# Optimization experiments

Measured on AMD Instinct MI355X. Metric: run time of the kernel, lower is better.

## Reference

```python
import math
import jax, jax.numpy as jnp
import numpy as np

B, T, D, V, S, R = 128, 32, 64, 4096, 32, 8
PONDER = 0.01
TWO_PI = np.float32(2.0 * math.pi)


def _ln(x, g, b, eps=1e-5):
    mu = x.mean(-1, keepdims=True)
    var = ((x - mu) ** 2).mean(-1, keepdims=True)
    return (x - mu) / jnp.sqrt(var + eps) * g + b


def _clin(xr, xi, Wr, br, Wi, bi):
    # ComplexLinear: fc_real/fc_imag share biases per torch module
    real = (xr @ Wr + br) - (xi @ Wi + bi)
    imag = (xi @ Wr + br) + (xr @ Wi + bi)
    return real, imag


def setup_inputs() -> dict:
    key = jax.random.key(0)
    ks = jax.random.split(key, 10)
    f = lambda k, sh, s: jax.random.normal(k, sh, jnp.float32) * s
    return {
        "x_seq": jax.random.randint(ks[0], (B, T), 0, V),
        "enc_emb": f(ks[1], (V, 2 * D), 0.02),
        "vq_emb": f(ks[2], (V, 2 * D), 0.05),
        "norm_rg": jnp.ones((D,), jnp.float32),
        "norm_rb": jnp.zeros((D,), jnp.float32),
        "norm_ig": jnp.ones((D,), jnp.float32),
        "norm_ib": jnp.zeros((D,), jnp.float32),
        "proj_w": f(ks[3], (3, 2, D, D), 0.05),  # [q/k/v, real/imag, in, out]
        "proj_b": f(ks[4], (3, 2, D), 0.01),
        "mem_gate_w": f(ks[5], (2 * D, 1), 0.05),
        "mem_gate_b": jnp.zeros((1,), jnp.float32),
        "arb_w": f(ks[6], (2 * D, 3), 0.05),
        "arb_b": jnp.zeros((3,), jnp.float32),
        "dec_w": f(ks[7], (2 * D, V), 0.02),
        "dec_b": jnp.zeros((V,), jnp.float32),
        "halt_bias": jnp.array(3.0, jnp.float32),
        "input_gate": jnp.array(0.0, jnp.float32),
    }


def _fwd(x_seq, enc_emb, vq_emb, norm_rg, norm_rb, norm_ig, norm_ib,
         proj_w, proj_b, mem_gate_w, mem_gate_b, arb_w, arb_b,
         dec_w, dec_b, halt_bias, input_gate):
    sg = jax.lax.stop_gradient
    emb = enc_emb[x_seq]                         # [B,T,2D]
    er, ei = emb[..., :D], emb[..., D:]
    alpha = jax.nn.sigmoid(input_gate)
    bias = jax.nn.softplus(halt_bias)
    vq_sq = (vq_emb ** 2).sum(-1)                # [V]

    def step(carry, xs):
        gw_r, gw_i, mem_r, mem_i = carry
        x_r, x_i = xs
        gw_r = alpha * gw_r + (1.0 - alpha) * x_r
        gw_i = alpha * gw_i + (1.0 - alpha) * x_i
        active = jnp.ones((x_r.shape[0],), jnp.float32)
        acc_vq = jnp.zeros_like(active)
        acc_ppx = jnp.zeros_like(active)
        acc_ent = jnp.zeros_like(active)
        acc_pond = jnp.zeros_like(active)
        acc_ph = jnp.zeros_like(active)
        prev_ang = jnp.arctan2(gw_i, gw_r)
        for _ in range(R):
            cr = _ln(gw_r, norm_rg, norm_rb)
            ci = _ln(gw_i, norm_ig, norm_ib)
            flat = jnp.concatenate([cr, ci], -1)            # [B,2D]
            # VQ (argmin over squared euclidean == argmin over cdist)
            d2 = (flat ** 2).sum(-1, keepdims=True) - 2.0 * (flat @ vq_emb.T) + vq_sq
            idx = jnp.argmin(d2, -1)                        # [B]
            zq = vq_emb[idx]                                # [B,2D]
            vq_loss = ((zq - sg(flat)) ** 2).mean(-1) + 0.25 * ((sg(zq) - flat) ** 2).mean(-1)
            zq_st = flat + sg(zq - flat)                    # straight-through
            avg = jax.nn.one_hot(idx, V, dtype=jnp.float32).mean(0)
            ent = -(avg * jnp.log(avg + 1e-10)).sum()
            ppx = jnp.exp(ent)
            vq_r, vq_i = zq_st[:, :D], zq_st[:, D:]
            # Hermitian gating
            qr, qi = _clin(cr, ci, proj_w[0, 0], proj_b[0, 0], proj_w[0, 1], proj_b[0, 1])
            kr, ki = _clin(cr, ci, proj_w[1, 0], proj_b[1, 0], proj_w[1, 1], proj_b[1, 1])
            wr, wi = _clin(cr, ci, proj_w[2, 0], proj_b[2, 0], proj_w[2, 1], proj_b[2, 1])
            gate = jax.nn.sigmoid((qr * kr + qi * ki).sum(-1, keepdims=True))
            g_r, g_i = wr * gate, wi * gate
            # memory read (mem unchanged during recursion)
            sim = jnp.einsum('bsd,bd->bs', mem_r, cr) + jnp.einsum('bsd,bd->bs', mem_i, ci)
            attn = jax.nn.softmax(sim, -1)
            m_r = jnp.einsum('bs,bsd->bd', attn, mem_r)
            m_i = jnp.einsum('bs,bsd->bd', attn, mem_i)
            # arbitrator mix
            gates = jax.nn.softmax(flat @ arb_w + arb_b, -1)  # [B,3]
            u_r = gates[:, 0:1] * g_r + gates[:, 1:2] * m_r + gates[:, 2:3] * vq_r
            u_i = gates[:, 0:1] * g_i + gates[:, 1:2] * m_i + gates[:, 2:3] * vq_i
            c_r = 0.6 * cr + 0.4 * u_r
            c_i = 0.6 * ci + 0.4 * u_i
            ang = jnp.arctan2(c_i, c_r)
            diff = jnp.abs(ang - prev_ang)
            diff = jnp.minimum(diff, TWO_PI - diff)
            acc_ph = acc_ph + active * diff.mean(-1)
            prev_ang = ang
            halt = jax.nn.sigmoid(bias - vq_loss)
            stop = (halt > 0.5).astype(jnp.float32)
            acc_pond = acc_pond + active * PONDER
            m = active > 0.5
            acc_vq = jnp.where(m, vq_loss, acc_vq)
            acc_ppx = jnp.where(m, ppx, acc_ppx)
            acc_ent = jnp.where(m, ent, acc_ent)
            gw_r = jnp.where(m[:, None], c_r, gw_r)
            gw_i = jnp.where(m[:, None], c_i, gw_i)
            active = active * (1.0 - stop)
        # final memory write (read output discarded, matching torch)
        flat_gw = jnp.concatenate([gw_r, gw_i], -1)
        wg = jax.nn.sigmoid(flat_gw @ mem_gate_w + mem_gate_b)  # [B,1]
        sh_r = jnp.roll(mem_r, 1, axis=1)
        sh_i = jnp.roll(mem_i, 1, axis=1)
        mem_r = sh_r.at[:, 0].set(wg * gw_r + (1.0 - wg) * sh_r[:, 0])
        mem_i = sh_i.at[:, 0].set(wg * gw_i + (1.0 - wg) * sh_i[:, 0])
        stats = jnp.stack([acc_vq.mean(), acc_ppx.mean(), acc_ent.mean(),
                           acc_pond.mean(), acc_ph.mean()])
        return (gw_r, gw_i, mem_r, mem_i), (gw_r, gw_i, stats)

    init = (jnp.zeros((B, D), jnp.float32), jnp.zeros((B, D), jnp.float32),
            jnp.zeros((B, S, D), jnp.float32), jnp.zeros((B, S, D), jnp.float32))
    xs = (jnp.moveaxis(er, 1, 0), jnp.moveaxis(ei, 1, 0))
    (gw_r, gw_i, mem_r, mem_i), (o_r, o_i, stats) = jax.lax.scan(step, init, xs)
    flat_out = jnp.concatenate([jnp.moveaxis(o_r, 0, 1), jnp.moveaxis(o_i, 0, 1)], -1)  # [B,T,2D]
    logits = flat_out @ dec_w + dec_b
    return logits, stats.mean(0), mem_r, mem_i


def reference(x_seq, enc_emb, vq_emb, norm_rg, norm_rb, norm_ig, norm_ib,
              proj_w, proj_b, mem_gate_w, mem_gate_b, arb_w, arb_b,
              dec_w, dec_b, halt_bias, input_gate):
    return _fwd(x_seq, enc_emb, vq_emb, norm_rg, norm_rb, norm_ig, norm_ib,
                proj_w, proj_b, mem_gate_w, mem_gate_b, arb_w, arb_b,
                dec_w, dec_b, halt_bias, input_gate)
```

## Files before the change

### kernel.cpp

```cpp
#include <hip/hip_runtime.h>
#include <math.h>

#define BB 128
#define TT 32
#define DDIM 64
#define VV 4096
#define SS 32
#define RR 8
#define NT 512
#define SMP 65

typedef unsigned short u16;
typedef unsigned int u32;
typedef _Float16 h2 __attribute__((ext_vector_type(2)));

__device__ __forceinline__ h2 bch(u32 u){ union { u32 u; h2 h; } v; v.u = u; return v.h; }

__device__ __forceinline__ float fdot2f(u32 a, u32 b, float acc){
#if __has_builtin(__builtin_amdgcn_fdot2)
  return __builtin_amdgcn_fdot2(bch(a), bch(b), acc, false);
#else
  h2 x = bch(a), y = bch(b);
  return acc + (float)x[0] * (float)y[0] + (float)x[1] * (float)y[1];
#endif
}

__device__ __forceinline__ u32 packh2(float a, float b){
  union { _Float16 h[2]; u32 u; } p;
  p.h[0] = (_Float16)a; p.h[1] = (_Float16)b;
  return p.u;
}

__global__ __launch_bounds__(256) void k_pack(const float* __restrict__ vq, u32* __restrict__ vqT){
  int gid = blockIdx.x * 256 + threadIdx.x;
  int l   = gid & 63;
  int dc8 = (gid >> 6) & 15;
  int c0  = gid >> 10;
  int c   = (c0 << 6) + l;
  const float* s = vq + c * 128 + dc8 * 8;
  uint4 o;
  o.x = packh2(s[0], s[1]);
  o.y = packh2(s[2], s[3]);
  o.z = packh2(s[4], s[5]);
  o.w = packh2(s[6], s[7]);
  ((uint4*)vqT)[gid] = o;
}

__global__ __launch_bounds__(256) void k_vqsq(const float* __restrict__ vq, float* __restrict__ vqsq){
  int c = blockIdx.x * 256 + threadIdx.x;
  float s = 0.f;
  for (int d = 0; d < 128; d++){ float v = vq[c * 128 + d]; s = fmaf(v, v, s); }
  vqsq[c] = s;
}

__global__ __launch_bounds__(NT) void k_recur(
    const int* __restrict__ x_seq, const float* __restrict__ enc_emb,
    const float* __restrict__ vq_emb, const u32* __restrict__ vqT,
    const float* __restrict__ vq_sq,
    const float* __restrict__ nrg, const float* __restrict__ nrb,
    const float* __restrict__ nig, const float* __restrict__ nib,
    const float* __restrict__ proj_w, const float* __restrict__ proj_b,
    const float* __restrict__ mgw, const float* __restrict__ mgb,
    const float* __restrict__ arb_w, const float* __restrict__ arb_b,
    const float* __restrict__ hb, const float* __restrict__ ig,
    float* __restrict__ gwout, float* __restrict__ flatF,
    int* __restrict__ idxbuf, int* __restrict__ rstop_g, float* __restrict__ accs,
    float* __restrict__ out_mem)
{
  const int b = blockIdx.x;
  const int tid = threadIdx.x;
  const int lane = tid & 63;
  const int wave = tid >> 6;

  __shared__ __align__(16) float s_gw[128];
  __shared__ __align__(16) float s_flat[128];
  __shared__ __align__(16) u32   s_flath[64];
  __shared__ float s_zq[128];
  __shared__ float s_c[128];
  __shared__ float s_mem[2][SS][SMP];
  __shared__ float s_mv[12][DDIM];
  __shared__ float s_qkw[6][DDIM];
  __shared__ float s_sim[SS];
  __shared__ float s_red[16];
  __shared__ float s_sc[4];
  __shared__ int   s_imin;
  __shared__ float s_cand[8];
  __shared__ int   s_candi[8];

  for (int i = tid; i < 128; i += NT) s_gw[i] = 0.f;
  for (int i = tid; i < 2 * SS * SMP; i += NT) ((float*)s_mem)[i] = 0.f;
  __syncthreads();

  const float alpha = 1.f / (1.f + expf(-ig[0]));
  float bias_h; { float x = hb[0]; bias_h = log1pf(expf(x)); }
  int head = 0;
  float prev_ang = 0.f;

  for (int t = 0; t < TT; t++){
    int xid = x_seq[b * TT + t];
    if (tid < 128){
      float e = enc_emb[xid * 128 + tid];
      s_gw[tid] = alpha * s_gw[tid] + (1.f - alpha) * e;
    }
    __syncthreads();
    if (wave == 0) prev_ang = atan2f(s_gw[64 + lane], s_gw[lane]);

    float acc_ph = 0.f, acc_vq = 0.f;
    int rst = 0;

    for (int r = 0; r < RR; r++){
      if (wave < 2){
        float x = s_gw[wave * 64 + lane];
        float mu = x;
        for (int m = 1; m < 64; m <<= 1) mu += __shfl_xor(mu, m);
        mu *= (1.f / 64.f);
        float dxl = x - mu;
        float vv = dxl * dxl;
        for (int m = 1; m < 64; m <<= 1) vv += __shfl_xor(vv, m);
        vv *= (1.f / 64.f);
        float rs = 1.f / sqrtf(vv + 1e-5f);
        const float* g  = wave ? nig : nrg;
        const float* bb = wave ? nib : nrb;
        float fv = dxl * rs * g[lane] + bb[lane];
        s_flat[wave * 64 + lane] = fv;
        float pv = __shfl_xor(fv, 1);
        if ((lane & 1) == 0)
          s_flath[(wave * 64 + lane) >> 1] = packh2(fv, pv);
      }
      __syncthreads();

      uint4 F[16];
      {
        const uint4* sfh4 = (const uint4*)s_flath;
        #pragma unroll
        for (int i = 0; i < 16; i++) F[i] = sfh4[i];
      }
      float bsc = 3.4e38f; int bidx = 0;
      #pragma unroll 1
      for (int k = 0; k < 8; k++){
        int c0 = wave + 8 * k;
        const uint4* vp = ((const uint4*)vqT) + (c0 * 16) * 64 + lane;
        uint4 U[16];
        #pragma unroll
        for (int dc8 = 0; dc8 < 16; dc8++) U[dc8] = vp[dc8 * 64];
        float dot = 0.f;
        #pragma unroll
        for (int dc8 = 0; dc8 < 16; dc8++){
          dot = fdot2f(U[dc8].x, F[dc8].x, dot);
          dot = fdot2f(U[dc8].y, F[dc8].y, dot);
          dot = fdot2f(U[dc8].z, F[dc8].z, dot);
          dot = fdot2f(U[dc8].w, F[dc8].w, dot);
        }
        int c = c0 * 64 + lane;
        float sc = vq_sq[c] - 2.f * dot;
        if (sc < bsc || (sc == bsc && c < bidx)){ bsc = sc; bidx = c; }
      }
      for (int m = 1; m < 64; m <<= 1){
        float os = __shfl_xor(bsc, m);
        int   oi = __shfl_xor(bidx, m);
        if (os < bsc || (os == bsc && oi < bidx)){ bsc = os; bidx = oi; }
      }
      if (lane == 0){ s_cand[wave] = bsc; s_candi[wave] = bidx; }
      __syncthreads();
      if (tid == 0){
        float bs = s_cand[0]; int bi = s_candi[0];
        for (int w = 1; w < 8; w++){
          float os = s_cand[w]; int oi = s_candi[w];
          if (os < bs || (os == bs && oi < bi)){ bs = os; bi = oi; }
        }
        s_imin = bi;
        idxbuf[(b * TT + t) * RR + r] = bi;
      }
      __syncthreads();
      int imin = s_imin;

      if (tid < 128){
        float z = vq_emb[imin * 128 + tid];
        s_zq[tid] = z;
        float dv = z - s_flat[tid];
        float sq = dv * dv;
        for (int m = 1; m < 64; m <<= 1) sq += __shfl_xor(sq, m);
        if (lane == 0) s_red[wave] = sq;
      }
      for (int mm = wave; mm < 12; mm += 8){
        int p = mm >> 2, kind = mm & 3;
        int xoff = (kind == 0 || kind == 3) ? 0 : 64;
        int wsel = (kind == 0 || kind == 2) ? 0 : 1;
        const float* W = proj_w + ((p * 2 + wsel) << 12);
        const float4* fx = (const float4*)&s_flat[xoff];
        float a = 0.f;
        #pragma unroll
        for (int i = 0; i < 16; i++){
          float4 fv = fx[i];
          a = fmaf(fv.x, W[(4 * i + 0) * 64 + lane], a);
          a = fmaf(fv.y, W[(4 * i + 1) * 64 + lane], a);
          a = fmaf(fv.z, W[(4 * i + 2) * 64 + lane], a);
          a = fmaf(fv.w, W[(4 * i + 3) * 64 + lane], a);
        }
        s_mv[mm][lane] = a;
      }
      __syncthreads();

      if (tid == 0) s_sc[1] = 1.25f * (s_red[0] + s_red[1]) * (1.f / 128.f);
      if (tid < 192){
        int p = tid >> 6, j = tid & 63;
        float A  = s_mv[p * 4 + 0][j];
        float Bv = s_mv[p * 4 + 1][j];
        float C  = s_mv[p * 4 + 2][j];
        float Dv = s_mv[p * 4 + 3][j];
        float br = proj_b[(p * 2 + 0) * 64 + j];
        float bi = proj_b[(p * 2 + 1) * 64 + j];
        s_qkw[p * 2 + 0][j] = A + br - Bv - bi;
        s_qkw[p * 2 + 1][j] = C + br + Dv + bi;
      }
      __syncthreads();

      if (wave == 0){
        float g = s_qkw[0][lane] * s_qkw[2][lane] + s_qkw[1][lane] * s_qkw[3][lane];
        for (int m = 1; m < 64; m <<= 1) g += __shfl_xor(g, m);
        if (lane == 0) s_sc[0] = 1.f / (1.f + expf(-g));
      }
      {
        int slot = tid >> 4, sub = tid & 15;
        float p = 0.f;
        for (int k = 0; k < 8; k++){
          int dd = sub * 8 + k;
          float mv = (dd < 64) ? s_mem[0][slot][dd] : s_mem[1][slot][dd - 64];
          p = fmaf(mv, s_flat[dd], p);
        }
        for (int m = 1; m < 16; m <<= 1) p += __shfl_xor(p, m, 16);
        if (sub == 0) s_sim[slot] = p;
      }
      __syncthreads();
      if (wave == 0 && lane < 32){
        float v = s_sim[lane];
        float mx = v;
        for (int m = 1; m < 32; m <<= 1) mx = fmaxf(mx, __shfl_xor(mx, m, 32));
        float e = expf(v - mx);
        float sm = e;
        for (int m = 1; m < 32; m <<= 1) sm += __shfl_xor(sm, m, 32);
        s_sim[lane] = e / sm;
      }
      __syncthreads();
      float m_reg = 0.f;
      if (tid < 128){
        int h = tid >> 6, d0 = tid & 63;
        for (int s2 = 0; s2 < 32; s2++)
          m_reg = fmaf(s_sim[s2], s_mem[h][s2][d0], m_reg);
      } else if (wave >= 2 && wave < 5){
        int k = wave - 2;
        float p = s_flat[lane] * arb_w[lane * 3 + k]
                + s_flat[64 + lane] * arb_w[(64 + lane) * 3 + k];
        for (int m = 1; m < 64; m <<= 1) p += __shfl_xor(p, m);
        if (lane == 0) s_red[4 + k] = p + arb_b[k];
      }
      __syncthreads();
      if (tid < 128){
        float l0 = s_red[4], l1 = s_red[5], l2 = s_red[6];
        float mx = fmaxf(l0, fmaxf(l1, l2));
        float e0 = expf(l0 - mx), e1 = expf(l1 - mx), e2 = expf(l2 - mx);
        float inv = 1.f / (e0 + e1 + e2);
        float g0 = e0 * inv, g1 = e1 * inv, g2 = e2 * inv;
        float gate = s_sc[0];
        int h = tid >> 6, j = tid & 63;
        float wv = s_qkw[4 + h][j];
        float u = g0 * (gate * wv) + g1 * m_reg + g2 * s_zq[tid];
        s_c[tid] = 0.6f * s_flat[tid] + 0.4f * u;
      }
      __syncthreads();
      if (wave == 0){
        float ang = atan2f(s_c[64 + lane], s_c[lane]);
        float df = fabsf(ang - prev_ang);
        df = fminf(df, 6.28318530717958647692f - df);
        prev_ang = ang;
        for (int m = 1; m < 64; m <<= 1) df += __shfl_xor(df, m);
        if (lane == 0) s_red[7] = df * (1.f / 64.f);
      }
      __syncthreads();
      float vl = s_sc[1];
      acc_ph += s_red[7];
      acc_vq = vl;
      rst = r;
      bool stop = (bias_h - vl) > 0.f;
      if (tid < 128) s_gw[tid] = s_c[tid];
      __syncthreads();
      if (stop) break;
    }

    float pond = 0.01f * (float)(rst + 1);
    if (tid < 128) gwout[(b * TT + t) * 128 + tid] = s_gw[tid];
    if (rst < RR - 1 && wave < 2){
      float x = s_gw[wave * 64 + lane];
      float mu = x;
      for (int m = 1; m < 64; m <<= 1) mu += __shfl_xor(mu, m);
      mu *= (1.f / 64.f);
      float dxl = x - mu;
      float vv = dxl * dxl;
      for (int m = 1; m < 64; m <<= 1) vv += __shfl_xor(vv, m);
      vv *= (1.f / 64.f);
      float rs = 1.f / sqrtf(vv + 1e-5f);
      const float* g  = wave ? nig : nrg;
      const float* bb = wave ? nib : nrb;
      flatF[(b * TT + t) * 128 + wave * 64 + lane] = dxl * rs * g[lane] + bb[lane];
    }
    if (wave < 2){
      float p = s_gw[wave * 64 + lane] * mgw[wave * 64 + lane];
      for (int m = 1; m < 64; m <<= 1) p += __shfl_xor(p, m);
      if (lane == 0) s_red[8 + wave] = p;
    }
    __syncthreads();
    float wg = 1.f / (1.f + expf(-(s_red[8] + s_red[9] + mgb[0])));
    head = (head + SS - 1) & (SS - 1);
    if (tid < 128){
      int h = tid >> 6, d0 = tid & 63;
      float old = s_mem[h][head][d0];
      s_mem[h][head][d0] = wg * s_gw[tid] + (1.f - wg) * old;
    }
    if (tid == 0){
      int o = b * TT + t;
      rstop_g[o] = rst;
      accs[o * 4 + 0] = acc_vq;
      accs[o * 4 + 1] = pond;
      accs[o * 4 + 2] = acc_ph;
    }
    __syncthreads();
  }

  for (int i = tid; i < SS * DDIM; i += NT){
    int s2 = i >> 6, d0 = i & 63;
    int ph = (head + s2) & (SS - 1);
    out_mem[b * SS * DDIM + i] = s_mem[0][ph][d0];
    out_mem[BB * SS * DDIM + b * SS * DDIM + i] = s_mem[1][ph][d0];
  }
}

__global__ void k_max(const int* __restrict__ rstop_g, int* __restrict__ maxr){
  int t = threadIdx.x;
  if (t >= TT) return;
  int mx = 0;
  for (int b = 0; b < BB; b++) mx = max(mx, rstop_g[b * TT + t]);
  maxr[t] = mx;
}

__global__ __launch_bounds__(256) void k_tail(
    const u32* __restrict__ vqT, const float* __restrict__ vq_sq,
    const float* __restrict__ flatF, const int* __restrict__ rstop_g,
    const int* __restrict__ maxr, int* __restrict__ idxbuf)
{
  int o = blockIdx.x;
  int t = o & (TT - 1);
  int rs = rstop_g[o];
  if (rs >= maxr[t]) return;
  __shared__ __align__(16) float sf[128];
  __shared__ __align__(16) u32 sfh[64];
  __shared__ float s_cand[4];
  __shared__ int   s_candi[4];
  int tid = threadIdx.x, lane = tid & 63, wave = tid >> 6;
  if (tid < 128) sf[tid] = flatF[o * 128 + tid];
  __syncthreads();
  if (tid < 64) sfh[tid] = packh2(sf[2 * tid], sf[2 * tid + 1]);
  __syncthreads();
  uint4 F[16];
  {
    const uint4* sfh4 = (const uint4*)sfh;
    #pragma unroll
    for (int i = 0; i < 16; i++) F[i] = sfh4[i];
  }
  float bsc = 3.4e38f; int bidx = 0;
  #pragma unroll 1
  for (int k = 0; k < 16; k++){
    int c0 = wave + 4 * k;
    const uint4* vp = ((const uint4*)vqT) + (c0 * 16) * 64 + lane;
    uint4 U[16];
    #pragma unroll
    for (int dc8 = 0; dc8 < 16; dc8++) U[dc8] = vp[dc8 * 64];
    float dot = 0.f;
    #pragma unroll
    for (int dc8 = 0; dc8 < 16; dc8++){
      dot = fdot2f(U[dc8].x, F[dc8].x, dot);
      dot = fdot2f(U[dc8].y, F[dc8].y, dot);
      dot = fdot2f(U[dc8].z, F[dc8].z, dot);
      dot = fdot2f(U[dc8].w, F[dc8].w, dot);
    }
    int c = c0 * 64 + lane;
    float sc = vq_sq[c] - 2.f * dot;
    if (sc < bsc || (sc == bsc && c < bidx)){ bsc = sc; bidx = c; }
  }
  for (int m = 1; m < 64; m <<= 1){
    float os = __shfl_xor(bsc, m);
    int   oi = __shfl_xor(bidx, m);
    if (os < bsc || (os == bsc && oi < bidx)){ bsc = os; bidx = oi; }
  }
  if (lane == 0){ s_cand[wave] = bsc; s_candi[wave] = bidx; }
  __syncthreads();
  if (tid == 0){
    float bs = s_cand[0]; int bi = s_candi[0];
    for (int w = 1; w < 4; w++){
      float os = s_cand[w]; int oi = s_candi[w];
      if (os < bs || (os == bs && oi < bi)){ bs = os; bi = oi; }
    }
    for (int r = rs + 1; r < RR; r++) idxbuf[o * RR + r] = bi;
  }
}

__global__ __launch_bounds__(512) void k_stats(
    const int* __restrict__ idxbuf, const int* __restrict__ rstop_g,
    const float* __restrict__ accs, const int* __restrict__ maxr,
    float* __restrict__ out_stats)
{
  __shared__ float s_ent[TT][RR];
  __shared__ int   s_vals[8][128];
  __shared__ float s_fin[8][5];
  int tid = threadIdx.x, lane = tid & 63, wave = tid >> 6;

  for (int base = 0; base < TT * RR; base += 8){
    int p = base + wave;
    int r = p >> 5, t = p & 31;
    bool act = (r <= maxr[t]);
    s_vals[wave][lane]      = idxbuf[(lane * TT + t) * RR + r];
    s_vals[wave][64 + lane] = idxbuf[((64 + lane) * TT + t) * RR + r];
    __syncthreads();
    if (act){
      int mine1 = s_vals[wave][lane], mine2 = s_vals[wave][64 + lane];
      int c1 = 0, c2 = 0;
      for (int j = 0; j < 128; j++){
        int v = s_vals[wave][j];
        c1 += (v == mine1); c2 += (v == mine2);
      }
      float contrib = -(logf((float)c1 * (1.f / 128.f) + 1e-10f)
                      + logf((float)c2 * (1.f / 128.f) + 1e-10f)) * (1.f / 128.f);
      for (int m = 1; m < 64; m <<= 1) contrib += __shfl_xor(contrib, m);
      if (lane == 0) s_ent[t][r] = contrib;
    }
    __syncthreads();
  }

  float sv = 0.f, sp = 0.f, se = 0.f, sn = 0.f, sh = 0.f;
  for (int o = tid; o < BB * TT; o += 512){
    int t = o & 31;
    int rs = rstop_g[o];
    float ent = s_ent[t][rs];
    se += ent;
    sp += expf(ent);
    sv += accs[o * 4 + 0];
    sn += accs[o * 4 + 1];
    sh += accs[o * 4 + 2];
  }
  for (int m = 1; m < 64; m <<= 1){
    sv += __shfl_xor(sv, m); sp += __shfl_xor(sp, m); se += __shfl_xor(se, m);
    sn += __shfl_xor(sn, m); sh += __shfl_xor(sh, m);
  }
  if (lane == 0){
    s_fin[wave][0] = sv; s_fin[wave][1] = sp; s_fin[wave][2] = se;
    s_fin[wave][3] = sn; s_fin[wave][4] = sh;
  }
  __syncthreads();
  if (tid == 0){
    float a[5] = {0.f, 0.f, 0.f, 0.f, 0.f};
    for (int w = 0; w < 8; w++)
      for (int j = 0; j < 5; j++) a[j] += s_fin[w][j];
    float inv = 1.f / (float)(BB * TT);
    for (int j = 0; j < 5; j++) out_stats[j] = a[j] * inv;
  }
}

__global__ __launch_bounds__(256) void k_dec(
    const float* __restrict__ gwout, const float* __restrict__ dec_w,
    const float* __restrict__ dec_b, float* __restrict__ out)
{
  __shared__ float At[32][128];
  int tid = threadIdx.x;
  int row0 = blockIdx.y * 32;
  int col0 = blockIdx.x * 256;
  {
    const float4* src = (const float4*)(gwout + row0 * 128);
    float4* dst = (float4*)&At[0][0];
    for (int i = tid; i < 1024; i += 256) dst[i] = src[i];
  }
  __syncthreads();
  int v = col0 + tid;
  float acc[32];
  #pragma unroll
  for (int r2 = 0; r2 < 32; r2++) acc[r2] = 0.f;
  for (int k = 0; k < 128; k += 4){
    float w0 = dec_w[(k + 0) * 4096 + v];
    float w1 = dec_w[(k + 1) * 4096 + v];
    float w2 = dec_w[(k + 2) * 4096 + v];
    float w3 = dec_w[(k + 3) * 4096 + v];
    #pragma unroll
    for (int r2 = 0; r2 < 32; r2++){
      float4 a = *(const float4*)&At[r2][k];
      acc[r2] = fmaf(a.x, w0, fmaf(a.y, w1, fmaf(a.z, w2, fmaf(a.w, w3, acc[r2]))));
    }
  }
  float bv = dec_b[v];
  for (int r2 = 0; r2 < 32; r2++)
    out[(row0 + r2) * 4096 + v] = acc[r2] + bv;
}

extern "C" void kernel_launch(void* const* d_in, const int* in_sizes, int n_in,
                              void* d_out, int out_size, void* d_ws, size_t ws_size,
                              hipStream_t stream){
  const int*   x_seq   = (const int*)  d_in[0];
  const float* enc_emb = (const float*)d_in[1];
  const float* vq_emb  = (const float*)d_in[2];
  const float* nrg     = (const float*)d_in[3];
  const float* nrb     = (const float*)d_in[4];
  const float* nig     = (const float*)d_in[5];
  const float* nib     = (const float*)d_in[6];
  const float* proj_w  = (const float*)d_in[7];
  const float* proj_b  = (const float*)d_in[8];
  const float* mgw     = (const float*)d_in[9];
  const float* mgb     = (const float*)d_in[10];
  const float* arb_w   = (const float*)d_in[11];
  const float* arb_b   = (const float*)d_in[12];
  const float* dec_w   = (const float*)d_in[13];
  const float* dec_b   = (const float*)d_in[14];
  const float* hb      = (const float*)d_in[15];
  const float* ig      = (const float*)d_in[16];

  char* ws = (char*)d_ws;
  u32*   vqT    = (u32*)  (ws + 0);
  float* vqsq   = (float*)(ws + 2097152);
  float* gwout  = (float*)(ws + 2113536);
  float* flatF  = (float*)(ws + 4210688);
  int*   idxbuf = (int*)  (ws + 6307840);
  int*   rstop  = (int*)  (ws + 6438912);
  float* accs   = (float*)(ws + 6455296);
  int*   maxr   = (int*)  (ws + 6520832);

  float* out = (float*)d_out;
  float* out_stats = out + 16777216;
  float* out_mem   = out + 16777221;

  k_pack <<<dim3(256), dim3(256), 0, stream>>>(vq_emb, vqT);
  k_vqsq <<<dim3(16),  dim3(256), 0, stream>>>(vq_emb, vqsq);
  k_recur<<<dim3(BB),  dim3(NT),  0, stream>>>(
      x_seq, enc_emb, vq_emb, vqT, vqsq,
      nrg, nrb, nig, nib, proj_w, proj_b, mgw, mgb, arb_w, arb_b, hb, ig,
      gwout, flatF, idxbuf, rstop, accs, out_mem);
  k_dec  <<<dim3(16, 128), dim3(256), 0, stream>>>(gwout, dec_w, dec_b, out);
  k_max  <<<dim3(1),   dim3(64),  0, stream>>>(rstop, maxr);
  k_tail <<<dim3(BB * TT), dim3(256), 0, stream>>>(vqT, vqsq, flatF, rstop, maxr, idxbuf);
  k_stats<<<dim3(1),   dim3(512), 0, stream>>>(idxbuf, rstop, accs, maxr, out_stats);
}
```

Measured before the change: 718.0 us.

## Restructure recurrent step: fewer barriers, prefetched codebook loads, fused projection phases

Restructures the inner ponder loop of the recurrent kernel so that the complex projections, memory-similarity softmax, arbitration logits and VQ loss run in parallel waves within a single phase. This cuts the number of block-wide barriers per iteration. Codebook loads are double-buffered in registers (Ua/Ub prefetch) and the dot products are split across several accumulators to hide memory latency. The normalized flat vector is no longer written out; the tail kernel recomputes the layer norm from gwout instead. In exchange, register pressure goes up and the merged phase depends on wave specialization being correct.

```diff
diff --git a/kernel.cpp b/kernel.cpp
--- a/kernel.cpp
+++ b/kernel.cpp
@@ -30,6 +30,8 @@
   p.h[0] = (_Float16)a; p.h[1] = (_Float16)b;
   return p.u;
 }
+
+__device__ __forceinline__ void bar(){ __syncthreads(); }
 
 __global__ __launch_bounds__(256) void k_pack(const float* __restrict__ vq, u32* __restrict__ vqT){
   int gid = blockIdx.x * 256 + threadIdx.x;
@@ -53,6 +55,26 @@
   vqsq[c] = s;
 }
 
+__device__ __forceinline__ void load8(uint4 (&U)[8], const uint4* vp){
+  #pragma unroll
+  for (int j = 0; j < 8; j++) U[j] = vp[j * 64];
+}
+
+__device__ __forceinline__ void dot8(const uint4 (&U)[8], const uint4 (&F)[16], int off,
+                                     float& a0, float& a1, float& a2, float& a3){
+  #pragma unroll
+  for (int j = 0; j < 8; j += 4){
+    a0 = fdot2f(U[j+0].x, F[off+j+0].x, a0); a0 = fdot2f(U[j+0].y, F[off+j+0].y, a0);
+    a0 = fdot2f(U[j+0].z, F[off+j+0].z, a0); a0 = fdot2f(U[j+0].w, F[off+j+0].w, a0);
+    a1 = fdot2f(U[j+1].x, F[off+j+1].x, a1); a1 = fdot2f(U[j+1].y, F[off+j+1].y, a1);
+    a1 = fdot2f(U[j+1].z, F[off+j+1].z, a1); a1 = fdot2f(U[j+1].w, F[off+j+1].w, a1);
+    a2 = fdot2f(U[j+2].x, F[off+j+2].x, a2); a2 = fdot2f(U[j+2].y, F[off+j+2].y, a2);
+    a2 = fdot2f(U[j+2].z, F[off+j+2].z, a2); a2 = fdot2f(U[j+2].w, F[off+j+2].w, a2);
+    a3 = fdot2f(U[j+3].x, F[off+j+3].x, a3); a3 = fdot2f(U[j+3].y, F[off+j+3].y, a3);
+    a3 = fdot2f(U[j+3].z, F[off+j+3].z, a3); a3 = fdot2f(U[j+3].w, F[off+j+3].w, a3);
+  }
+}
+
 __global__ __launch_bounds__(NT) void k_recur(
     const int* __restrict__ x_seq, const float* __restrict__ enc_emb,
     const float* __restrict__ vq_emb, const u32* __restrict__ vqT,
@@ -63,7 +85,7 @@
     const float* __restrict__ mgw, const float* __restrict__ mgb,
     const float* __restrict__ arb_w, const float* __restrict__ arb_b,
     const float* __restrict__ hb, const float* __restrict__ ig,
-    float* __restrict__ gwout, float* __restrict__ flatF,
+    float* __restrict__ gwout,
     int* __restrict__ idxbuf, int* __restrict__ rstop_g, float* __restrict__ accs,
     float* __restrict__ out_mem)
 {
@@ -75,15 +97,11 @@
   __shared__ __align__(16) float s_gw[128];
   __shared__ __align__(16) float s_flat[128];
   __shared__ __align__(16) u32   s_flath[64];
-  __shared__ float s_zq[128];
-  __shared__ float s_c[128];
+  __shared__ __align__(16) float s_c[128];
   __shared__ float s_mem[2][SS][SMP];
-  __shared__ float s_mv[12][DDIM];
-  __shared__ float s_qkw[6][DDIM];
+  __shared__ __align__(16) float s_qkw[6][DDIM];
   __shared__ float s_sim[SS];
-  __shared__ float s_red[16];
-  __shared__ float s_sc[4];
-  __shared__ int   s_imin;
+  __shared__ float s_red[8];
   __shared__ float s_cand[8];
   __shared__ int   s_candi[8];
 
@@ -96,26 +114,37 @@
   int head = 0;
   float prev_ang = 0.f;
 
+  const uint4* vqT4 = (const uint4*)vqT;
+
+  #pragma unroll 1
   for (int t = 0; t < TT; t++){
     int xid = x_seq[b * TT + t];
+
+    uint4 Ua[8], Ub[8];
+    load8(Ua, vqT4 + (wave * 16) * 64 + lane);
+
     if (tid < 128){
       float e = enc_emb[xid * 128 + tid];
       s_gw[tid] = alpha * s_gw[tid] + (1.f - alpha) * e;
     }
-    __syncthreads();
+    bar();
     if (wave == 0) prev_ang = atan2f(s_gw[64 + lane], s_gw[lane]);
 
-    float acc_ph = 0.f, acc_vq = 0.f;
+    float acc_ph = 0.f, vl_last = 0.f;
     int rst = 0;
-
+    bool stop = false;
+
+    #pragma unroll 1
     for (int r = 0; r < RR; r++){
       if (wave < 2){
         float x = s_gw[wave * 64 + lane];
         float mu = x;
+        #pragma unroll
         for (int m = 1; m < 64; m <<= 1) mu += __shfl_xor(mu, m);
         mu *= (1.f / 64.f);
         float dxl = x - mu;
         float vv = dxl * dxl;
+        #pragma unroll
         for (int m = 1; m < 64; m <<= 1) vv += __shfl_xor(vv, m);
         vv *= (1.f / 64.f);
         float rs = 1.f / sqrtf(vv + 1e-5f);
@@ -127,205 +156,189 @@
         if ((lane & 1) == 0)
           s_flath[(wave * 64 + lane) >> 1] = packh2(fv, pv);
       }
-      __syncthreads();
+      bar();
 
       uint4 F[16];
       {
         const uint4* sfh4 = (const uint4*)s_flath;
         #pragma unroll
-        for (int i = 0; i < 16; i++) F[i] = sfh4[i];
-      }
+        for (int j = 0; j < 16; j++) F[j] = sfh4[j];
+      }
+      if (r > 0) load8(Ua, vqT4 + (wave * 16) * 64 + lane);
+      load8(Ub, vqT4 + (wave * 16 + 8) * 64 + lane);
+      float Q[8];
+      #pragma unroll
+      for (int k = 0; k < 8; k++) Q[k] = vq_sq[((wave + 8 * k) << 6) + lane];
+
       float bsc = 3.4e38f; int bidx = 0;
-      #pragma unroll 1
+      #pragma unroll
       for (int k = 0; k < 8; k++){
-        int c0 = wave + 8 * k;
-        const uint4* vp = ((const uint4*)vqT) + (c0 * 16) * 64 + lane;
-        uint4 U[16];
-        #pragma unroll
-        for (int dc8 = 0; dc8 < 16; dc8++) U[dc8] = vp[dc8 * 64];
-        float dot = 0.f;
-        #pragma unroll
-        for (int dc8 = 0; dc8 < 16; dc8++){
-          dot = fdot2f(U[dc8].x, F[dc8].x, dot);
-          dot = fdot2f(U[dc8].y, F[dc8].y, dot);
-          dot = fdot2f(U[dc8].z, F[dc8].z, dot);
-          dot = fdot2f(U[dc8].w, F[dc8].w, dot);
-        }
-        int c = c0 * 64 + lane;
-        float sc = vq_sq[c] - 2.f * dot;
+        float a0 = 0.f, a1 = 0.f, a2 = 0.f, a3 = 0.f;
+        dot8(Ua, F, 0, a0, a1, a2, a3);
+        if (k < 7) load8(Ua, vqT4 + ((wave + 8 * (k + 1)) * 16) * 64 + lane);
+        dot8(Ub, F, 8, a0, a1, a2, a3);
+        if (k < 7) load8(Ub, vqT4 + ((wave + 8 * (k + 1)) * 16 + 8) * 64 + lane);
+        float dot = (a0 + a1) + (a2 + a3);
+        int c = ((wave + 8 * k) << 6) + lane;
+        float sc = Q[k] - 2.f * dot;
         if (sc < bsc || (sc == bsc && c < bidx)){ bsc = sc; bidx = c; }
       }
+      #pragma unroll
       for (int m = 1; m < 64; m <<= 1){
         float os = __shfl_xor(bsc, m);
         int   oi = __shfl_xor(bidx, m);
         if (os < bsc || (os == bsc && oi < bidx)){ bsc = os; bidx = oi; }
       }
       if (lane == 0){ s_cand[wave] = bsc; s_candi[wave] = bidx; }
-      __syncthreads();
-      if (tid == 0){
+      bar();
+
+      int imin = 0;
+      if (wave < 2){
         float bs = s_cand[0]; int bi = s_candi[0];
+        #pragma unroll
         for (int w = 1; w < 8; w++){
           float os = s_cand[w]; int oi = s_candi[w];
           if (os < bs || (os == bs && oi < bi)){ bs = os; bi = oi; }
         }
-        s_imin = bi;
-        idxbuf[(b * TT + t) * RR + r] = bi;
-      }
-      __syncthreads();
-      int imin = s_imin;
+        imin = __builtin_amdgcn_readfirstlane(bi);
+      }
+
+      if (wave >= 2){
+        const int w2 = wave - 2;
+        const int p = w2 >> 1, ri = w2 & 1;
+        const float* Wr = proj_w + ((p * 2 + 0) << 12);
+        const float* Wi = proj_w + ((p * 2 + 1) << 12);
+        const float* xA = s_flat + (ri ? 64 : 0);
+        const float* xB = s_flat + (ri ? 0 : 64);
+        float a0=0.f,a1=0.f,a2=0.f,a3=0.f, b0=0.f,b1=0.f,b2=0.f,b3=0.f;
+        #pragma unroll
+        for (int i = 0; i < 64; i += 4){
+          float4 xv = *(const float4*)&xA[i];
+          a0 = fmaf(xv.x, Wr[(i + 0) * 64 + lane], a0);
+          a1 = fmaf(xv.y, Wr[(i + 1) * 64 + lane], a1);
+          a2 = fmaf(xv.z, Wr[(i + 2) * 64 + lane], a2);
+          a3 = fmaf(xv.w, Wr[(i + 3) * 64 + lane], a3);
+        }
+        #pragma unroll
+        for (int i = 0; i < 64; i += 4){
+          float4 xv = *(const float4*)&xB[i];
+          b0 = fmaf(xv.x, Wi[(i + 0) * 64 + lane], b0);
+          b1 = fmaf(xv.y, Wi[(i + 1) * 64 + lane], b1);
+          b2 = fmaf(xv.z, Wi[(i + 2) * 64 + lane], b2);
+          b3 = fmaf(xv.w, Wi[(i + 3) * 64 + lane], b3);
+        }
+        float A  = (a0 + a1) + (a2 + a3);
+        float Bv = (b0 + b1) + (b2 + b3);
+        float br  = proj_b[(p * 2 + 0) * 64 + lane];
+        float bi2 = proj_b[(p * 2 + 1) * 64 + lane];
+        s_qkw[w2][lane] = ri ? (A + Bv + br + bi2) : (A - Bv + br - bi2);
+      } else if (wave == 0){
+        const int s2 = lane & 31, h = lane >> 5;
+        const float* mrow = &s_mem[h][s2][0];
+        const float* fx = s_flat + h * 64;
+        float a0=0.f,a1=0.f,a2=0.f,a3=0.f;
+        #pragma unroll
+        for (int d = 0; d < 64; d += 4){
+          a0 = fmaf(mrow[d + 0], fx[d + 0], a0);
+          a1 = fmaf(mrow[d + 1], fx[d + 1], a1);
+          a2 = fmaf(mrow[d + 2], fx[d + 2], a2);
+          a3 = fmaf(mrow[d + 3], fx[d + 3], a3);
+        }
+        float p = (a0 + a1) + (a2 + a3);
+        p += __shfl_xor(p, 32);
+        float mx = p;
+        #pragma unroll
+        for (int m = 1; m < 32; m <<= 1) mx = fmaxf(mx, __shfl_xor(mx, m));
+        float e = expf(p - mx);
+        float sm = e;
+        #pragma unroll
+        for (int m = 1; m < 32; m <<= 1) sm += __shfl_xor(sm, m);
+        if (lane < 32) s_sim[lane] = e / sm;
+      } else {
+        float f0 = s_flat[lane], f1 = s_flat[64 + lane];
+        float p0 = fmaf(f0, arb_w[lane * 3 + 0], f1 * arb_w[(64 + lane) * 3 + 0]);
+        float p1 = fmaf(f0, arb_w[lane * 3 + 1], f1 * arb_w[(64 + lane) * 3 + 1]);
+        float p2 = fmaf(f0, arb_w[lane * 3 + 2], f1 * arb_w[(64 + lane) * 3 + 2]);
+        float z0 = vq_emb[imin * 128 + lane];
+        float z1 = vq_emb[imin * 128 + 64 + lane];
+        float d0 = z0 - f0, d1 = z1 - f1;
+        float sq = d0 * d0 + d1 * d1;
+        #pragma unroll
+        for (int m = 1; m < 64; m <<= 1){
+          p0 += __shfl_xor(p0, m); p1 += __shfl_xor(p1, m);
+          p2 += __shfl_xor(p2, m); sq += __shfl_xor(sq, m);
+        }
+        if (lane == 0){
+          s_red[4] = p0 + arb_b[0];
+          s_red[5] = p1 + arb_b[1];
+          s_red[6] = p2 + arb_b[2];
+          s_red[0] = 1.25f * sq * (1.f / 128.f);
+          idxbuf[(b * TT + t) * RR + r] = imin;
+        }
+      }
+      bar();
+
+      float vl = s_red[0];
+      stop = (bias_h - vl) > 0.f;
+      vl_last = vl; rst = r;
 
       if (tid < 128){
-        float z = vq_emb[imin * 128 + tid];
-        s_zq[tid] = z;
-        float dv = z - s_flat[tid];
-        float sq = dv * dv;
-        for (int m = 1; m < 64; m <<= 1) sq += __shfl_xor(sq, m);
-        if (lane == 0) s_red[wave] = sq;
-      }
-      for (int mm = wave; mm < 12; mm += 8){
-        int p = mm >> 2, kind = mm & 3;
-        int xoff = (kind == 0 || kind == 3) ? 0 : 64;
-        int wsel = (kind == 0 || kind == 2) ? 0 : 1;
-        const float* W = proj_w + ((p * 2 + wsel) << 12);
-        const float4* fx = (const float4*)&s_flat[xoff];
-        float a = 0.f;
-        #pragma unroll
-        for (int i = 0; i < 16; i++){
-          float4 fv = fx[i];
-          a = fmaf(fv.x, W[(4 * i + 0) * 64 + lane], a);
-          a = fmaf(fv.y, W[(4 * i + 1) * 64 + lane], a);
-          a = fmaf(fv.z, W[(4 * i + 2) * 64 + lane], a);
-          a = fmaf(fv.w, W[(4 * i + 3) * 64 + lane], a);
-        }
-        s_mv[mm][lane] = a;
-      }
-      __syncthreads();
-
-      if (tid == 0) s_sc[1] = 1.25f * (s_red[0] + s_red[1]) * (1.f / 128.f);
-      if (tid < 192){
-        int p = tid >> 6, j = tid & 63;
-        float A  = s_mv[p * 4 + 0][j];
-        float Bv = s_mv[p * 4 + 1][j];
-        float C  = s_mv[p * 4 + 2][j];
-        float Dv = s_mv[p * 4 + 3][j];
-        float br = proj_b[(p * 2 + 0) * 64 + j];
-        float bi = proj_b[(p * 2 + 1) * 64 + j];
-        s_qkw[p * 2 + 0][j] = A + br - Bv - bi;
-        s_qkw[p * 2 + 1][j] = C + br + Dv + bi;
-      }
-      __syncthreads();
-
-      if (wave == 0){
-        float g = s_qkw[0][lane] * s_qkw[2][lane] + s_qkw[1][lane] * s_qkw[3][lane];
+        float g = fmaf(s_qkw[0][lane], s_qkw[2][lane], s_qkw[1][lane] * s_qkw[3][lane]);
+        #pragma unroll
         for (int m = 1; m < 64; m <<= 1) g += __shfl_xor(g, m);
-        if (lane == 0) s_sc[0] = 1.f / (1.f + expf(-g));
-      }
-      {
-        int slot = tid >> 4, sub = tid & 15;
-        float p = 0.f;
-        for (int k = 0; k < 8; k++){
-          int dd = sub * 8 + k;
-          float mv = (dd < 64) ? s_mem[0][slot][dd] : s_mem[1][slot][dd - 64];
-          p = fmaf(mv, s_flat[dd], p);
-        }
-        for (int m = 1; m < 16; m <<= 1) p += __shfl_xor(p, m, 16);
-        if (sub == 0) s_sim[slot] = p;
-      }
-      __syncthreads();
-      if (wave == 0 && lane < 32){
-        float v = s_sim[lane];
-        float mx = v;
-        for (int m = 1; m < 32; m <<= 1) mx = fmaxf(mx, __shfl_xor(mx, m, 32));
-        float e = expf(v - mx);
-        float sm = e;
-        for (int m = 1; m < 32; m <<= 1) sm += __shfl_xor(sm, m, 32);
-        s_sim[lane] = e / sm;
-      }
-      __syncthreads();
-      float m_reg = 0.f;
-      if (tid < 128){
-        int h = tid >> 6, d0 = tid & 63;
+        float gate = 1.f / (1.f + expf(-g));
+        const int h = wave, j = lane;
+        float m_reg = 0.f;
+        #pragma unroll 8
         for (int s2 = 0; s2 < 32; s2++)
-          m_reg = fmaf(s_sim[s2], s_mem[h][s2][d0], m_reg);
-      } else if (wave >= 2 && wave < 5){
-        int k = wave - 2;
-        float p = s_flat[lane] * arb_w[lane * 3 + k]
-                + s_flat[64 + lane] * arb_w[(64 + lane) * 3 + k];
-        for (int m = 1; m < 64; m <<= 1) p += __shfl_xor(p, m);
-        if (lane == 0) s_red[4 + k] = p + arb_b[k];
-      }
-      __syncthreads();
-      if (tid < 128){
+          m_reg = fmaf(s_sim[s2], s_mem[h][s2][j], m_reg);
         float l0 = s_red[4], l1 = s_red[5], l2 = s_red[6];
         float mx = fmaxf(l0, fmaxf(l1, l2));
         float e0 = expf(l0 - mx), e1 = expf(l1 - mx), e2 = expf(l2 - mx);
         float inv = 1.f / (e0 + e1 + e2);
-        float g0 = e0 * inv, g1 = e1 * inv, g2 = e2 * inv;
-        float gate = s_sc[0];
-        int h = tid >> 6, j = tid & 63;
+        float zq = vq_emb[imin * 128 + tid];
         float wv = s_qkw[4 + h][j];
-        float u = g0 * (gate * wv) + g1 * m_reg + g2 * s_zq[tid];
-        s_c[tid] = 0.6f * s_flat[tid] + 0.4f * u;
-      }
-      __syncthreads();
+        float u = (e0 * inv) * (gate * wv) + (e1 * inv) * m_reg + (e2 * inv) * zq;
+        float cv = 0.6f * s_flat[tid] + 0.4f * u;
+        s_c[tid]  = cv;
+        s_gw[tid] = cv;
+      }
+      bar();
+
       if (wave == 0){
         float ang = atan2f(s_c[64 + lane], s_c[lane]);
         float df = fabsf(ang - prev_ang);
         df = fminf(df, 6.28318530717958647692f - df);
         prev_ang = ang;
+        #pragma unroll
         for (int m = 1; m < 64; m <<= 1) df += __shfl_xor(df, m);
-        if (lane == 0) s_red[7] = df * (1.f / 64.f);
-      }
-      __syncthreads();
-      float vl = s_sc[1];
-      acc_ph += s_red[7];
-      acc_vq = vl;
-      rst = r;
-      bool stop = (bias_h - vl) > 0.f;
-      if (tid < 128) s_gw[tid] = s_c[tid];
-      __syncthreads();
+        acc_ph += df * (1.f / 64.f);
+      }
       if (stop) break;
     }
 
     float pond = 0.01f * (float)(rst + 1);
     if (tid < 128) gwout[(b * TT + t) * 128 + tid] = s_gw[tid];
-    if (rst < RR - 1 && wave < 2){
-      float x = s_gw[wave * 64 + lane];
-      float mu = x;
-      for (int m = 1; m < 64; m <<= 1) mu += __shfl_xor(mu, m);
-      mu *= (1.f / 64.f);
-      float dxl = x - mu;
-      float vv = dxl * dxl;
-      for (int m = 1; m < 64; m <<= 1) vv += __shfl_xor(vv, m);
-      vv *= (1.f / 64.f);
-      float rs = 1.f / sqrtf(vv + 1e-5f);
-      const float* g  = wave ? nig : nrg;
-      const float* bb = wave ? nib : nrb;
-      flatF[(b * TT + t) * 128 + wave * 64 + lane] = dxl * rs * g[lane] + bb[lane];
-    }
+    head = (head + SS - 1) & (SS - 1);
     if (wave < 2){
-      float p = s_gw[wave * 64 + lane] * mgw[wave * 64 + lane];
+      float p = fmaf(s_c[lane], mgw[lane], s_c[64 + lane] * mgw[64 + lane]);
+      #pragma unroll
       for (int m = 1; m < 64; m <<= 1) p += __shfl_xor(p, m);
-      if (lane == 0) s_red[8 + wave] = p;
-    }
-    __syncthreads();
-    float wg = 1.f / (1.f + expf(-(s_red[8] + s_red[9] + mgb[0])));
-    head = (head + SS - 1) & (SS - 1);
-    if (tid < 128){
-      int h = tid >> 6, d0 = tid & 63;
+      float wg = 1.f / (1.f + expf(-(p + mgb[0])));
+      const int h = wave, d0 = lane;
       float old = s_mem[h][head][d0];
-      s_mem[h][head][d0] = wg * s_gw[tid] + (1.f - wg) * old;
+      s_mem[h][head][d0] = wg * s_c[h * 64 + d0] + (1.f - wg) * old;
     }
     if (tid == 0){
       int o = b * TT + t;
       rstop_g[o] = rst;
-      accs[o * 4 + 0] = acc_vq;
+      accs[o * 4 + 0] = vl_last;
       accs[o * 4 + 1] = pond;
       accs[o * 4 + 2] = acc_ph;
     }
-    __syncthreads();
-  }
-
+  }
+
+  bar();
   for (int i = tid; i < SS * DDIM; i += NT){
     int s2 = i >> 6, d0 = i & 63;
     int ph = (head + s2) & (SS - 1);
@@ -344,21 +357,37 @@
 
 __global__ __launch_bounds__(256) void k_tail(
     const u32* __restrict__ vqT, const float* __restrict__ vq_sq,
-    const float* __restrict__ flatF, const int* __restrict__ rstop_g,
-    const int* __restrict__ maxr, int* __restrict__ idxbuf)
+    const float* __restrict__ gwout, const int* __restrict__ rstop_g,
+    const int* __restrict__ maxr, int* __restrict__ idxbuf,
+    const float* __restrict__ nrg, const float* __restrict__ nrb,
+    const float* __restrict__ nig, const float* __restrict__ nib)
 {
   int o = blockIdx.x;
   int t = o & (TT - 1);
   int rs = rstop_g[o];
   if (rs >= maxr[t]) return;
-  __shared__ __align__(16) float sf[128];
   __shared__ __align__(16) u32 sfh[64];
   __shared__ float s_cand[4];
   __shared__ int   s_candi[4];
   int tid = threadIdx.x, lane = tid & 63, wave = tid >> 6;
-  if (tid < 128) sf[tid] = flatF[o * 128 + tid];
-  __syncthreads();
-  if (tid < 64) sfh[tid] = packh2(sf[2 * tid], sf[2 * tid + 1]);
+  if (wave < 2){
+    float x = gwout[o * 128 + wave * 64 + lane];
+    float mu = x;
+    #pragma unroll
+    for (int m = 1; m < 64; m <<= 1) mu += __shfl_xor(mu, m);
+    mu *= (1.f / 64.f);
+    float dxl = x - mu;
+    float vv = dxl * dxl;
+    #pragma unroll
+    for (int m = 1; m < 64; m <<= 1) vv += __shfl_xor(vv, m);
+    vv *= (1.f / 64.f);
+    float rsn = 1.f / sqrtf(vv + 1e-5f);
+    const float* g  = wave ? nig : nrg;
+    const float* bb = wave ? nib : nrb;
+    float fv = dxl * rsn * g[lane] + bb[lane];
+    float pv = __shfl_xor(fv, 1);
+    if ((lane & 1) == 0) sfh[(wave * 64 + lane) >> 1] = packh2(fv, pv);
+  }
   __syncthreads();
   uint4 F[16];
   {
@@ -386,6 +415,7 @@
     float sc = vq_sq[c] - 2.f * dot;
     if (sc < bsc || (sc == bsc && c < bidx)){ bsc = sc; bidx = c; }
   }
+  #pragma unroll
   for (int m = 1; m < 64; m <<= 1){
     float os = __shfl_xor(bsc, m);
     int   oi = __shfl_xor(bidx, m);
@@ -523,7 +553,6 @@
   u32*   vqT    = (u32*)  (ws + 0);
   float* vqsq   = (float*)(ws + 2097152);
   float* gwout  = (float*)(ws + 2113536);
-  float* flatF  = (float*)(ws + 4210688);
   int*   idxbuf = (int*)  (ws + 6307840);
   int*   rstop  = (int*)  (ws + 6438912);
   float* accs   = (float*)(ws + 6455296);
@@ -538,9 +567,10 @@
   k_recur<<<dim3(BB),  dim3(NT),  0, stream>>>(
       x_seq, enc_emb, vq_emb, vqT, vqsq,
       nrg, nrb, nig, nib, proj_w, proj_b, mgw, mgb, arb_w, arb_b, hb, ig,
-      gwout, flatF, idxbuf, rstop, accs, out_mem);
+      gwout, idxbuf, rstop, accs, out_mem);
   k_dec  <<<dim3(16, 128), dim3(256), 0, stream>>>(gwout, dec_w, dec_b, out);
   k_max  <<<dim3(1),   dim3(64),  0, stream>>>(rstop, maxr);
-  k_tail <<<dim3(BB * TT), dim3(256), 0, stream>>>(vqT, vqsq, flatF, rstop, maxr, idxbuf);
+  k_tail <<<dim3(BB * TT), dim3(256), 0, stream>>>(vqT, vqsq, gwout, rstop, maxr, idxbuf,
+                                                   nrg, nrb, nig, nib);
   k_stats<<<dim3(1),   dim3(512), 0, stream>>>(idxbuf, rstop, accs, maxr, out_stats);
 }
```

Result: slower. 2.124 ms (+195.9%).
